# Kernel tuning notes

Hardware: AMD Instinct MI355X
Metric: run time of the kernel (lower is better)

## Reference

```python
import jax, jax.numpy as jnp
import numpy as np

D, K, CIN, CD, COUT = 3, 16, 128, 32, 256
C = CIN + CD                  # 160 = C_in + C_delta after concat
DM = -(-COUT // C)            # depth_multiplier = ceil(C_out / C) = 2
N, I = 4, 2048                # batch, points per cloud; M = N*I = 8192


def _bn(x, g, b, eps=1e-5):
    # BatchNorm1d in training mode: biased batch statistics over dim 0
    mu = x.mean(0)
    v = x.var(0)
    return (x - mu) * jax.lax.rsqrt(v + eps) * g + b


def _knn(p, k):
    # knn_graph over ALL M points (wrapper passes no batch vector), loop=True
    d2 = jnp.sum(p * p, axis=1)
    dist = d2[:, None] + d2[None, :] - 2.0 * (p @ p.T)   # [M,M]
    _, idx = jax.lax.top_k(-dist, k)                     # [M,K], self first
    return idx


def _gconv(t, w, b, M):
    # grouped Conv1d(K, K*K, kernel=K, groups=K): t [M,K,K], w [K(cin), K(out/grp), K(tap)]
    return jnp.einsum('mcl,col->mco', t, w).reshape(M, K * K) + b


def _xconv(xf, pf, idx, w1a, b1a, g1a, be1a, w1b, b1b, g1b, be1b,
           w2, b2, g2a, be2a, wc2a, bc2a, g2b, be2b, wc2b, bc2b, g2c, be2c,
           wcd, bcd, wl, bl):
    M = pf.shape[0]
    rel = pf[idx] - pf[:, None, :]                       # [M,K,D] relative neighbor coords
    # mlp1: lift relative coords to C_delta features
    h = rel.reshape(M * K, D)
    h = _bn(jax.nn.elu(h @ w1a + b1a), g1a, be1a)
    h = _bn(jax.nn.elu(h @ w1b + b1b), g1b, be1b)
    x_star = jnp.concatenate([h.reshape(M, K, CD), xf[idx]], axis=-1)  # [M,K,C]
    x_star = x_star.transpose(0, 2, 1)                   # [M,C,K]
    # mlp2: learn KxK X-transformation from the K*D relative coords
    t = _bn(jax.nn.elu(rel.reshape(M, K * D) @ w2 + b2), g2a, be2a).reshape(M, K, K)
    t = _bn(jax.nn.elu(_gconv(t, wc2a, bc2a, M)), g2b, be2b).reshape(M, K, K)
    t = _bn(_gconv(t, wc2b, bc2b, M), g2c, be2c).reshape(M, K, K)
    xt = jnp.einsum('mck,mkj->mcj', x_star, t)           # [M,C,K] batched matmul
    # depthwise Conv1d(C, C*DM, K, groups=C) collapses K, then final Linear
    y = jnp.einsum('mcl,col->mco', xt, wcd).reshape(M, C * DM) + bcd
    return y @ wl + bl                                   # [M,COUT]


def setup_inputs() -> dict:
    key = jax.random.key(0)
    ks = jax.random.split(key, 16)
    r = lambda k, s: jax.random.normal(k, s, jnp.float32) * 0.1
    return dict(
        x=jax.random.normal(ks[0], (N, I, CIN), jnp.float32),
        pos=jax.random.normal(ks[1], (N, I, D), jnp.float32),
        w1a=r(ks[2], (D, CD)), b1a=r(ks[3], (CD,)), g1a=jnp.ones((CD,)), be1a=jnp.zeros((CD,)),
        w1b=r(ks[4], (CD, CD)), b1b=r(ks[5], (CD,)), g1b=jnp.ones((CD,)), be1b=jnp.zeros((CD,)),
        w2=r(ks[6], (D * K, K * K)), b2=r(ks[7], (K * K,)), g2a=jnp.ones((K * K,)), be2a=jnp.zeros((K * K,)),
        wc2a=r(ks[8], (K, K, K)), bc2a=r(ks[9], (K * K,)), g2b=jnp.ones((K * K,)), be2b=jnp.zeros((K * K,)),
        wc2b=r(ks[10], (K, K, K)), bc2b=r(ks[11], (K * K,)), g2c=jnp.ones((K * K,)), be2c=jnp.zeros((K * K,)),
        wcd=r(ks[12], (C, DM, K)), bcd=r(ks[13], (C * DM,)),
        wl=r(ks[14], (C * DM, COUT)), bl=r(ks[15], (COUT,)),
    )


def reference(x, pos, w1a, b1a, g1a, be1a, w1b, b1b, g1b, be1b,
              w2, b2, g2a, be2a, wc2a, bc2a, g2b, be2b, wc2b, bc2b, g2c, be2c,
              wcd, bcd, wl, bl):
    pf = pos.reshape(N * I, D)
    xf = x.reshape(N * I, CIN)
    idx = _knn(pf, K)
    out = _xconv(xf, pf, idx, w1a, b1a, g1a, be1a, w1b, b1b, g1b, be1b,
                 w2, b2, g2a, be2a, wc2a, bc2a, g2b, be2b, wc2b, bc2b, g2c, be2c,
                 wcd, bcd, wl, bl)
    return out.reshape(N, I, COUT)
```

## Files before the change

### kernel.cpp

```cpp
#include <hip/hip_runtime.h>
#include <math.h>

#define M_PTS 8192
#define MK    131072

__device__ __forceinline__ float elu(float v){ return v > 0.f ? v : __expf(v)-1.0f; }

__device__ __forceinline__ unsigned distkey(float4 c, float qx, float qy, float qz, float d2q){
  #pragma clang fp contract(off)
  float dot  = __builtin_fmaf(c.z, qz, __builtin_fmaf(c.y, qy, __builtin_fmaf(c.x, qx, 0.0f)));
  float A    = d2q + c.w;
  float B    = 2.0f * dot;
  float dist = A - B;
  unsigned u = __float_as_uint(dist);
  return u ^ ((unsigned)((int)u >> 31) | 0x80000000u);
}

__global__ __launch_bounds__(256) void knn_kernel(const float* __restrict__ pos,
                                                  int* __restrict__ nidx,
                                                  float* __restrict__ st){
  #pragma clang fp contract(off)
  __shared__ float4 cand[1024];
  __shared__ unsigned long long hits[4][64];
  int tid  = threadIdx.x;
  int lane = tid & 63;
  int wv   = tid >> 6;
  int q    = blockIdx.x*4 + wv;
  if (blockIdx.x == 0){
    for (int i = tid; i < 2048; i += 256) st[i] = 0.f;
  }
  float qx = pos[3*q], qy = pos[3*q+1], qz = pos[3*q+2];
  float d2q = (qx*qx + qy*qy) + qz*qz;

  unsigned ka[8];
  #pragma unroll
  for (int s=0;s<8;s++) ka[s] = 0xFFFFFFFFu;

  for (int base = 0; base < M_PTS; base += 1024){
    for (int t = tid; t < 1024; t += 256){
      int j = base + t;
      float x = pos[3*j], y = pos[3*j+1], z = pos[3*j+2];
      float d2v = (x*x + y*y) + z*z;
      cand[t] = make_float4(x,y,z,d2v);
    }
    __syncthreads();
    #pragma unroll
    for (int k=0; k<16; k++){
      unsigned v = distkey(cand[lane + k*64], qx, qy, qz, d2q);
      #pragma unroll
      for (int s=0;s<8;s++){
        unsigned mn = min(v, ka[s]);
        unsigned mx = max(v, ka[s]);
        ka[s] = mn; v = mx;
      }
    }
    __syncthreads();
  }

  unsigned thr = 0xFFFFFFFFu;
  for (int r=0; r<16; r++){
    unsigned mine = ka[0];
    unsigned best = mine;
    #pragma unroll
    for (int off=32; off>0; off>>=1){
      unsigned o = __shfl_xor(best, off, 64);
      best = min(best, o);
    }
    bool adv = (best == mine);
    #pragma unroll
    for (int s=0;s<7;s++) ka[s] = adv ? ka[s+1] : ka[s];
    ka[7] = adv ? 0xFFFFFFFFu : ka[7];
    thr = best;
  }

  int cnt = 0;
  for (int base = 0; base < M_PTS; base += 1024){
    for (int t = tid; t < 1024; t += 256){
      int j = base + t;
      float x = pos[3*j], y = pos[3*j+1], z = pos[3*j+2];
      float d2v = (x*x + y*y) + z*z;
      cand[t] = make_float4(x,y,z,d2v);
    }
    __syncthreads();
    #pragma unroll
    for (int k=0; k<16; k++){
      int j = base + lane + k*64;
      unsigned u = distkey(cand[lane + k*64], qx, qy, qz, d2q);
      bool hit = (u <= thr);
      unsigned long long m = __ballot(hit);
      if (hit){
        int slot = cnt + __popcll(m & ((1ull<<lane)-1ull));
        if (slot < 64) hits[wv][slot] = ((unsigned long long)u << 32) | (unsigned)j;
      }
      cnt += (int)__popcll(m);
    }
    __syncthreads();
  }

  int cc = min(cnt, 64);
  unsigned long long mine = (lane < cc) ? hits[wv][lane] : ~0ull;
  for (int r=0; r<16; r++){
    unsigned long long best = mine;
    #pragma unroll
    for (int off=32; off>0; off>>=1){
      unsigned long long o = __shfl_xor(best, off, 64);
      best = (o < best) ? o : best;
    }
    if (mine == best) mine = ~0ull;
    if (lane == 0) nidx[q*16 + r] = (int)(unsigned)best;
  }
}

#define COMPUTE_RELF_8(OFFS)                                          \
  for (int f = tid; f < 8*48; f += 256){                              \
    int p = f/48, kd = f%48, k = kd/3, d = kd%3;                      \
    int j = nidx[(m0+p)*16 + k];                                      \
    relf[p][kd] = pos[3*j+d] - pos[3*(m0+p)+d];                       \
  }                                                                   \
  __syncthreads();

#define COMPUTE_T1_8(acc)                                             \
  _Pragma("unroll")                                                   \
  for (int p=0;p<8;p++) acc[p] = b2[tid];                             \
  for (int kk=0; kk<48; kk++){                                        \
    float w = w2[kk*256 + tid];                                       \
    _Pragma("unroll")                                                 \
    for (int p=0;p<8;p++) acc[p] += relf[p][kk]*w;                    \
  }

__global__ __launch_bounds__(256) void stats_a_kernel(const float* __restrict__ pos,
    const int* __restrict__ nidx,
    const float* __restrict__ w1a, const float* __restrict__ b1a,
    const float* __restrict__ w2,  const float* __restrict__ b2,
    float* __restrict__ s1, float* __restrict__ s3){
  int tid = threadIdx.x;
  if (blockIdx.x < 512){
    __shared__ float relS[256][3];
    __shared__ float red[8][64];
    int r = blockIdx.x*256 + tid;
    int m = r >> 4;
    int j = nidx[r];
    relS[tid][0] = pos[3*j  ]-pos[3*m  ];
    relS[tid][1] = pos[3*j+1]-pos[3*m+1];
    relS[tid][2] = pos[3*j+2]-pos[3*m+2];
    __syncthreads();
    int c = tid & 31, g = tid >> 5;
    float w0=w1a[c], w1v=w1a[32+c], w2v=w1a[64+c], b=b1a[c];
    float s=0.f, q=0.f;
    for (int rr=g*32; rr<g*32+32; rr++){
      float h = elu(b + relS[rr][0]*w0 + relS[rr][1]*w1v + relS[rr][2]*w2v);
      s += h; q += h*h;
    }
    red[g][c]=s; red[g][32+c]=q;
    __syncthreads();
    if (tid < 64){
      float a=0.f;
      #pragma unroll
      for (int gg=0;gg<8;gg++) a += red[gg][tid];
      atomicAdd(&s1[tid], a);
    }
  } else {
    __shared__ float relf[8][48];
    int m0 = (blockIdx.x-512)*8;
    COMPUTE_RELF_8();
    float acc[8];
    COMPUTE_T1_8(acc);
    float s=0.f, q=0.f;
    #pragma unroll
    for (int p=0;p<8;p++){ float v = elu(acc[p]); s += v; q += v*v; }
    atomicAdd(&s3[tid], s); atomicAdd(&s3[256+tid], q);
  }
}

__global__ __launch_bounds__(256) void stats_b_kernel(const float* __restrict__ pos,
    const int* __restrict__ nidx,
    const float* __restrict__ w1a, const float* __restrict__ b1a,
    const float* __restrict__ s1,  const float* __restrict__ g1a, const float* __restrict__ be1a,
    const float* __restrict__ w1b, const float* __restrict__ b1b,
    const float* __restrict__ w2,  const float* __restrict__ b2,
    const float* __restrict__ s3,  const float* __restrict__ g2a, const float* __restrict__ be2a,
    const float* __restrict__ wc2a,const float* __restrict__ bc2a,
    float* __restrict__ s2, float* __restrict__ s4){
  int tid = threadIdx.x;
  const float invMK = 1.f/(float)MK;
  const float invM  = 1.f/8192.f;
  if (blockIdx.x < 2048){
    __shared__ float xnS[64][33];
    __shared__ float red[8][64];
    __shared__ float muA[32], ivA[32];
    if (tid < 32){
      float mu  = s1[tid]*invMK;
      float var = s1[32+tid]*invMK - mu*mu;
      muA[tid] = mu; ivA[tid] = rsqrtf(var+1e-5f)*g1a[tid];
    }
    __syncthreads();
    {
      int rl = tid >> 2;
      int r  = blockIdx.x*64 + rl;
      int m = r >> 4;
      int j = nidx[r];
      float rx = pos[3*j]-pos[3*m], ry = pos[3*j+1]-pos[3*m+1], rz = pos[3*j+2]-pos[3*m+2];
      int c0 = (tid & 3)*8;
      #pragma unroll
      for (int u=0; u<8; u++){
        int cc = c0 + u;
        float h = elu(b1a[cc] + rx*w1a[cc] + ry*w1a[32+cc] + rz*w1a[64+cc]);
        xnS[rl][cc] = (h-muA[cc])*ivA[cc] + be1a[cc];
      }
    }
    __syncthreads();
    int o = tid & 31, g = tid >> 5;
    float wcol[32];
    #pragma unroll
    for (int cc=0;cc<32;cc++) wcol[cc] = w1b[cc*32+o];
    float bo = b1b[o], s=0.f, q=0.f;
    for (int rr=g*8; rr<g*8+8; rr++){
      float a = bo;
      #pragma unroll
      for (int cc=0;cc<32;cc++) a += xnS[rr][cc]*wcol[cc];
      float v = elu(a);
      s += v; q += v*v;
    }
    red[g][o]=s; red[g][32+o]=q;
    __syncthreads();
    if (tid < 64){
      float a=0.f;
      #pragma unroll
      for (int gg=0;gg<8;gg++) a += red[gg][tid];
      atomicAdd(&s2[tid], a);
    }
  } else {
    __shared__ float relf[8][48];
    __shared__ float tn[8][256];
    int m0 = (blockIdx.x-2048)*8;
    COMPUTE_RELF_8();
    float acc[8];
    COMPUTE_T1_8(acc);
    float mu3  = s3[tid]*invM;
    float var3 = s3[256+tid]*invM - mu3*mu3;
    float i3   = rsqrtf(var3+1e-5f)*g2a[tid];
    float bb3  = be2a[tid];
    #pragma unroll
    for (int p=0;p<8;p++) tn[p][tid] = (elu(acc[p])-mu3)*i3 + bb3;
    __syncthreads();
    int c = tid >> 4;
    float wreg[16];
    const float4* wv4 = (const float4*)(wc2a + tid*16);
    #pragma unroll
    for (int v=0; v<4; v++){ float4 f = wv4[v]; wreg[4*v]=f.x; wreg[4*v+1]=f.y; wreg[4*v+2]=f.z; wreg[4*v+3]=f.w; }
    float bias = bc2a[tid];
    float s=0.f, q=0.f;
    #pragma unroll
    for (int p=0;p<8;p++){
      float a2 = bias;
      #pragma unroll
      for (int l=0;l<16;l++) a2 += tn[p][c*16+l]*wreg[l];
      float v = elu(a2);
      s += v; q += v*v;
    }
    atomicAdd(&s4[tid], s); atomicAdd(&s4[256+tid], q);
  }
}

__global__ __launch_bounds__(256) void t3_stats_kernel(const float* __restrict__ pos,
    const int* __restrict__ nidx, const float* __restrict__ w2, const float* __restrict__ b2,
    const float* __restrict__ s3, const float* __restrict__ g2a, const float* __restrict__ be2a,
    const float* __restrict__ wc2a, const float* __restrict__ bc2a,
    const float* __restrict__ s4, const float* __restrict__ g2b, const float* __restrict__ be2b,
    const float* __restrict__ wc2b, const float* __restrict__ bc2b, float* __restrict__ s5){
  __shared__ float relf[8][48];
  __shared__ float tn[8][256];
  __shared__ float tn2[8][256];
  int m0 = blockIdx.x*8, tid = threadIdx.x;
  const float invM = 1.f/8192.f;
  COMPUTE_RELF_8();
  float acc[8];
  COMPUTE_T1_8(acc);
  float mu3  = s3[tid]*invM;
  float var3 = s3[256+tid]*invM - mu3*mu3;
  float i3   = rsqrtf(var3+1e-5f)*g2a[tid];
  float bb3  = be2a[tid];
  #pragma unroll
  for (int p=0;p<8;p++) tn[p][tid] = (elu(acc[p])-mu3)*i3 + bb3;
  __syncthreads();
  int c = tid >> 4;
  float wreg[16];
  { const float4* wv4 = (const float4*)(wc2a + tid*16);
    #pragma unroll
    for (int v=0; v<4; v++){ float4 f = wv4[v]; wreg[4*v]=f.x; wreg[4*v+1]=f.y; wreg[4*v+2]=f.z; wreg[4*v+3]=f.w; } }
  float bias = bc2a[tid];
  float mu4  = s4[tid]*invM;
  float var4 = s4[256+tid]*invM - mu4*mu4;
  float i4   = rsqrtf(var4+1e-5f)*g2b[tid];
  float bb4  = be2b[tid];
  float t2v[8];
  #pragma unroll
  for (int p=0;p<8;p++){
    float a2 = bias;
    #pragma unroll
    for (int l=0;l<16;l++) a2 += tn[p][c*16+l]*wreg[l];
    t2v[p] = elu(a2);
  }
  #pragma unroll
  for (int p=0;p<8;p++) tn2[p][tid] = (t2v[p]-mu4)*i4 + bb4;
  __syncthreads();
  float w2reg[16];
  { const float4* wv4 = (const float4*)(wc2b + tid*16);
    #pragma unroll
    for (int v=0; v<4; v++){ float4 f = wv4[v]; w2reg[4*v]=f.x; w2reg[4*v+1]=f.y; w2reg[4*v+2]=f.z; w2reg[4*v+3]=f.w; } }
  float bias2 = bc2b[tid];
  float s=0.f, q=0.f;
  #pragma unroll
  for (int p=0;p<8;p++){
    float a3 = bias2;
    #pragma unroll
    for (int l=0;l<16;l++) a3 += tn2[p][c*16+l]*w2reg[l];
    s += a3; q += a3*a3;
  }
  atomicAdd(&s5[tid], s); atomicAdd(&s5[256+tid], q);
}

#define PF 4
__global__ __launch_bounds__(256) void final_kernel(
    const float* __restrict__ x, const float* __restrict__ pos, const int* __restrict__ nidx,
    const float* __restrict__ w1a, const float* __restrict__ b1a,
    const float* __restrict__ g1a, const float* __restrict__ be1a,
    const float* __restrict__ w1b, const float* __restrict__ b1b,
    const float* __restrict__ g1b, const float* __restrict__ be1b,
    const float* __restrict__ w2,  const float* __restrict__ b2,
    const float* __restrict__ g2a, const float* __restrict__ be2a,
    const float* __restrict__ wc2a,const float* __restrict__ bc2a,
    const float* __restrict__ g2b, const float* __restrict__ be2b,
    const float* __restrict__ wc2b,const float* __restrict__ bc2b,
    const float* __restrict__ g2c, const float* __restrict__ be2c,
    const float* __restrict__ wcd, const float* __restrict__ bcd,
    const float* __restrict__ wl,  const float* __restrict__ bl,
    const float* __restrict__ st,
    float* __restrict__ out){
  __shared__ float relf[PF][48];
  __shared__ float tA[PF][256];
  __shared__ float tB[PF][256];
  __shared__ float xs[PF*32*17];
  __shared__ float yy[PF][320];
  __shared__ int   sidx[PF*16];
  __shared__ float mu1[32], i1g[32], mu2[32], i2g[32];
  int tid = threadIdx.x;
  int m0  = blockIdx.x*PF;
  const float invMK = 1.f/(float)MK;
  const float invM  = 1.f/8192.f;

  if (tid < PF*16) sidx[tid] = nidx[m0*16 + tid];
  for (int f = tid; f < PF*48; f += 256){
    int p = f/48, kd = f%48, k = kd/3, d = kd%3;
    int j = nidx[(m0+p)*16 + k];
    relf[p][kd] = pos[3*j+d] - pos[3*(m0+p)+d];
  }
  if (tid < 32){
    float mu  = st[tid]*invMK;
    float var = st[32+tid]*invMK - mu*mu;
    mu1[tid] = mu; i1g[tid] = rsqrtf(var+1e-5f)*g1a[tid];
    float mu_2  = st[64+tid]*invMK;
    float var_2 = st[96+tid]*invMK - mu_2*mu_2;
    mu2[tid] = mu_2; i2g[tid] = rsqrtf(var_2+1e-5f)*g1b[tid];
  }
  float mu3 = st[128+tid]*invM, var3 = st[384+tid]*invM - mu3*mu3;
  float i3 = rsqrtf(var3+1e-5f)*g2a[tid], bb3 = be2a[tid];
  float mu4 = st[640+tid]*invM, var4 = st[896+tid]*invM - mu4*mu4;
  float i4 = rsqrtf(var4+1e-5f)*g2b[tid], bb4 = be2b[tid];
  float mu5 = st[1152+tid]*invM, var5 = st[1408+tid]*invM - mu5*mu5;
  float i5 = rsqrtf(var5+1e-5f)*g2c[tid], bb5 = be2c[tid];
  __syncthreads();

  {
    float a[PF];
    #pragma unroll
    for (int p=0;p<PF;p++) a[p] = b2[tid];
    for (int kk=0; kk<48; kk++){
      float w = w2[kk*256 + tid];
      #pragma unroll
      for (int p=0;p<PF;p++) a[p] += relf[p][kk]*w;
    }
    #pragma unroll
    for (int p=0;p<PF;p++) tA[p][tid] = (elu(a[p])-mu3)*i3 + bb3;
  }
  __syncthreads();

  int c = tid >> 4;
  {
    float wreg[16];
    const float4* wv4 = (const float4*)(wc2a + tid*16);
    #pragma unroll
    for (int v=0; v<4; v++){ float4 f = wv4[v]; wreg[4*v]=f.x; wreg[4*v+1]=f.y; wreg[4*v+2]=f.z; wreg[4*v+3]=f.w; }
    float bias = bc2a[tid];
    float t2v[PF];
    #pragma unroll
    for (int p=0;p<PF;p++){
      float a2 = bias;
      #pragma unroll
      for (int l=0;l<16;l++) a2 += tA[p][c*16+l]*wreg[l];
      t2v[p] = elu(a2);
    }
    #pragma unroll
    for (int p=0;p<PF;p++) tB[p][tid] = (t2v[p]-mu4)*i4 + bb4;
  }
  __syncthreads();

  {
    float w2reg[16];
    const float4* wv4 = (const float4*)(wc2b + tid*16);
    #pragma unroll
    for (int v=0; v<4; v++){ float4 f = wv4[v]; w2reg[4*v]=f.x; w2reg[4*v+1]=f.y; w2reg[4*v+2]=f.z; w2reg[4*v+3]=f.w; }
    float bias2 = bc2b[tid];
    #pragma unroll
    for (int p=0;p<PF;p++){
      float a3 = bias2;
      #pragma unroll
      for (int l=0;l<16;l++) a3 += tB[p][c*16+l]*w2reg[l];
      tA[p][tid] = (a3-mu5)*i5 + bb5;
    }
  }

  {
    int row = tid >> 2;
    int p = row >> 4, k = row & 15;
    int q8 = (tid & 3)*8;
    int m = m0 + p;
    int j = sidx[p*16 + k];
    float rx = pos[3*j]-pos[3*m], ry = pos[3*j+1]-pos[3*m+1], rz = pos[3*j+2]-pos[3*m+2];
    float xn[32];
    #pragma unroll
    for (int cc=0; cc<32; cc++){
      float h = elu(b1a[cc] + rx*w1a[cc] + ry*w1a[32+cc] + rz*w1a[64+cc]);
      xn[cc] = (h-mu1[cc])*i1g[cc] + be1a[cc];
    }
    #pragma unroll
    for (int oo=0; oo<8; oo++){
      int o = q8 + oo;
      float a = b1b[o];
      #pragma unroll
      for (int cc=0; cc<32; cc++) a += xn[cc]*w1b[cc*32+o];
      float h2v = elu(a);
      xs[(p*32 + o)*17 + k] = (h2v-mu2[o])*i2g[o] + be1b[o];
    }
  }
  __syncthreads();

  for (int pair = tid; pair < PF*160; pair += 256){
    int p = pair / 160, cch = pair % 160;
    float av[16];
    if (cch < 32){
      #pragma unroll
      for (int k16=0;k16<16;k16++) av[k16] = xs[(p*32+cch)*17 + k16];
    } else {
      #pragma unroll
      for (int k16=0;k16<16;k16++) av[k16] = x[(size_t)sidx[p*16+k16]*128 + (cch-32)];
    }
    float xt[16];
    #pragma unroll
    for (int j16=0;j16<16;j16++) xt[j16]=0.f;
    #pragma unroll
    for (int k16=0;k16<16;k16++){
      float a = av[k16];
      #pragma unroll
      for (int j16=0;j16<16;j16++) xt[j16] += a*tA[p][k16*16+j16];
    }
    float y0 = bcd[cch*2], y1 = bcd[cch*2+1];
    #pragma unroll
    for (int l=0;l<16;l++){
      y0 += xt[l]*wcd[cch*32 + l];
      y1 += xt[l]*wcd[cch*32 + 16 + l];
    }
    yy[p][cch*2] = y0; yy[p][cch*2+1] = y1;
  }
  __syncthreads();

  float accO[PF];
  #pragma unroll
  for (int p=0;p<PF;p++) accO[p] = bl[tid];
  for (int q=0;q<320;q++){
    float w = wl[q*256 + tid];
    #pragma unroll
    for (int p=0;p<PF;p++) accO[p] += yy[p][q]*w;
  }
  #pragma unroll
  for (int p=0;p<PF;p++) out[(size_t)(m0+p)*256 + tid] = accO[p];
}

extern "C" void kernel_launch(void* const* d_in, const int* in_sizes, int n_in,
                              void* d_out, int out_size, void* d_ws, size_t ws_size,
                              hipStream_t stream){
  const float* x    = (const float*)d_in[0];
  const float* pos  = (const float*)d_in[1];
  const float* w1a  = (const float*)d_in[2];
  const float* b1a  = (const float*)d_in[3];
  const float* g1a  = (const float*)d_in[4];
  const float* be1a = (const float*)d_in[5];
  const float* w1b  = (const float*)d_in[6];
  const float* b1b  = (const float*)d_in[7];
  const float* g1b  = (const float*)d_in[8];
  const float* be1b = (const float*)d_in[9];
  const float* w2   = (const float*)d_in[10];
  const float* b2   = (const float*)d_in[11];
  const float* g2a  = (const float*)d_in[12];
  const float* be2a = (const float*)d_in[13];
  const float* wc2a = (const float*)d_in[14];
  const float* bc2a = (const float*)d_in[15];
  const float* g2b  = (const float*)d_in[16];
  const float* be2b = (const float*)d_in[17];
  const float* wc2b = (const float*)d_in[18];
  const float* bc2b = (const float*)d_in[19];
  const float* g2c  = (const float*)d_in[20];
  const float* be2c = (const float*)d_in[21];
  const float* wcd  = (const float*)d_in[22];
  const float* bcd  = (const float*)d_in[23];
  const float* wl   = (const float*)d_in[24];
  const float* bl   = (const float*)d_in[25];
  float* out = (float*)d_out;

  char* ws = (char*)d_ws;
  int*   nidx = (int*)(ws + 0);
  float* st   = (float*)(ws + 524288);
  float* s1 = st;
  float* s2 = st + 64;
  float* s3 = st + 128;
  float* s4 = st + 640;
  float* s5 = st + 1152;

  knn_kernel<<<2048,256,0,stream>>>(pos, nidx, st);
  stats_a_kernel<<<1536,256,0,stream>>>(pos, nidx, w1a, b1a, w2, b2, s1, s3);
  stats_b_kernel<<<3072,256,0,stream>>>(pos, nidx, w1a, b1a, s1, g1a, be1a, w1b, b1b,
                                        w2, b2, s3, g2a, be2a, wc2a, bc2a, s2, s4);
  t3_stats_kernel<<<1024,256,0,stream>>>(pos, nidx, w2, b2, s3, g2a, be2a, wc2a, bc2a,
                                         s4, g2b, be2b, wc2b, bc2b, s5);
  final_kernel<<<2048,256,0,stream>>>(x, pos, nidx,
                                      w1a, b1a, g1a, be1a, w1b, b1b, g1b, be1b,
                                      w2, b2, g2a, be2a, wc2a, bc2a,
                                      g2b, be2b, wc2b, bc2b, g2c, be2c,
                                      wcd, bcd, wl, bl, st, out);
}
```

Before: 404.3 us.

## Vectorize loads across kernels and halve points per block in stats kernels

The kNN candidate staging now reads positions as float4 triples instead of scalar strided loads. The stats kernels handle 4 points per block instead of 8, doubling grid sizes to expose more parallelism. The w2 and wl matvec loops are unrolled by 4 with float4 shared-memory reads, and the final kernel's mlp1 path uses float4 weight loads with the 8 outputs accumulated together. The smaller blocks re-read weights more often and add more atomics on the statistics.

```diff
diff --git a/kernel.cpp b/kernel.cpp
--- a/kernel.cpp
+++ b/kernel.cpp
@@ -37,11 +37,13 @@
   for (int s=0;s<8;s++) ka[s] = 0xFFFFFFFFu;
 
   for (int base = 0; base < M_PTS; base += 1024){
-    for (int t = tid; t < 1024; t += 256){
-      int j = base + t;
-      float x = pos[3*j], y = pos[3*j+1], z = pos[3*j+2];
-      float d2v = (x*x + y*y) + z*z;
-      cand[t] = make_float4(x,y,z,d2v);
+    {
+      const float4* pv = (const float4*)(pos + (size_t)base*3);
+      float4 f0 = pv[3*tid], f1 = pv[3*tid+1], f2 = pv[3*tid+2];
+      cand[4*tid  ] = make_float4(f0.x,f0.y,f0.z,(f0.x*f0.x + f0.y*f0.y) + f0.z*f0.z);
+      cand[4*tid+1] = make_float4(f0.w,f1.x,f1.y,(f0.w*f0.w + f1.x*f1.x) + f1.y*f1.y);
+      cand[4*tid+2] = make_float4(f1.z,f1.w,f2.x,(f1.z*f1.z + f1.w*f1.w) + f2.x*f2.x);
+      cand[4*tid+3] = make_float4(f2.y,f2.z,f2.w,(f2.y*f2.y + f2.z*f2.z) + f2.w*f2.w);
     }
     __syncthreads();
     #pragma unroll
@@ -75,11 +77,13 @@
 
   int cnt = 0;
   for (int base = 0; base < M_PTS; base += 1024){
-    for (int t = tid; t < 1024; t += 256){
-      int j = base + t;
-      float x = pos[3*j], y = pos[3*j+1], z = pos[3*j+2];
-      float d2v = (x*x + y*y) + z*z;
-      cand[t] = make_float4(x,y,z,d2v);
+    {
+      const float4* pv = (const float4*)(pos + (size_t)base*3);
+      float4 f0 = pv[3*tid], f1 = pv[3*tid+1], f2 = pv[3*tid+2];
+      cand[4*tid  ] = make_float4(f0.x,f0.y,f0.z,(f0.x*f0.x + f0.y*f0.y) + f0.z*f0.z);
+      cand[4*tid+1] = make_float4(f0.w,f1.x,f1.y,(f0.w*f0.w + f1.x*f1.x) + f1.y*f1.y);
+      cand[4*tid+2] = make_float4(f1.z,f1.w,f2.x,(f1.z*f1.z + f1.w*f1.w) + f2.x*f2.x);
+      cand[4*tid+3] = make_float4(f2.y,f2.z,f2.w,(f2.y*f2.y + f2.z*f2.z) + f2.w*f2.w);
     }
     __syncthreads();
     #pragma unroll
@@ -111,21 +115,25 @@
   }
 }
 
-#define COMPUTE_RELF_8(OFFS)                                          \
-  for (int f = tid; f < 8*48; f += 256){                              \
+#define COMPUTE_RELF_4()                                              \
+  for (int f = tid; f < 4*48; f += 256){                              \
     int p = f/48, kd = f%48, k = kd/3, d = kd%3;                      \
     int j = nidx[(m0+p)*16 + k];                                      \
     relf[p][kd] = pos[3*j+d] - pos[3*(m0+p)+d];                       \
   }                                                                   \
   __syncthreads();
 
-#define COMPUTE_T1_8(acc)                                             \
+#define COMPUTE_T1_4(acc)                                             \
   _Pragma("unroll")                                                   \
-  for (int p=0;p<8;p++) acc[p] = b2[tid];                             \
-  for (int kk=0; kk<48; kk++){                                        \
-    float w = w2[kk*256 + tid];                                       \
+  for (int p=0;p<4;p++) acc[p] = b2[tid];                             \
+  for (int kk=0; kk<48; kk+=4){                                       \
+    float w0v = w2[kk*256+tid],     w1v = w2[(kk+1)*256+tid];         \
+    float w2v = w2[(kk+2)*256+tid], w3v = w2[(kk+3)*256+tid];         \
     _Pragma("unroll")                                                 \
-    for (int p=0;p<8;p++) acc[p] += relf[p][kk]*w;                    \
+    for (int p=0;p<4;p++){                                            \
+      float4 r4 = *(const float4*)&relf[p][kk];                       \
+      acc[p] += r4.x*w0v + r4.y*w1v + r4.z*w2v + r4.w*w3v;            \
+    }                                                                 \
   }
 
 __global__ __launch_bounds__(256) void stats_a_kernel(const float* __restrict__ pos,
@@ -160,14 +168,14 @@
       atomicAdd(&s1[tid], a);
     }
   } else {
-    __shared__ float relf[8][48];
-    int m0 = (blockIdx.x-512)*8;
-    COMPUTE_RELF_8();
-    float acc[8];
-    COMPUTE_T1_8(acc);
+    __shared__ float relf[4][48];
+    int m0 = (blockIdx.x-512)*4;
+    COMPUTE_RELF_4();
+    float acc[4];
+    COMPUTE_T1_4(acc);
     float s=0.f, q=0.f;
     #pragma unroll
-    for (int p=0;p<8;p++){ float v = elu(acc[p]); s += v; q += v*v; }
+    for (int p=0;p<4;p++){ float v = elu(acc[p]); s += v; q += v*v; }
     atomicAdd(&s3[tid], s); atomicAdd(&s3[256+tid], q);
   }
 }
@@ -230,18 +238,18 @@
       atomicAdd(&s2[tid], a);
     }
   } else {
-    __shared__ float relf[8][48];
-    __shared__ float tn[8][256];
-    int m0 = (blockIdx.x-2048)*8;
-    COMPUTE_RELF_8();
-    float acc[8];
-    COMPUTE_T1_8(acc);
+    __shared__ float relf[4][48];
+    __shared__ float tn[4][256];
+    int m0 = (blockIdx.x-2048)*4;
+    COMPUTE_RELF_4();
+    float acc[4];
+    COMPUTE_T1_4(acc);
     float mu3  = s3[tid]*invM;
     float var3 = s3[256+tid]*invM - mu3*mu3;
     float i3   = rsqrtf(var3+1e-5f)*g2a[tid];
     float bb3  = be2a[tid];
     #pragma unroll
-    for (int p=0;p<8;p++) tn[p][tid] = (elu(acc[p])-mu3)*i3 + bb3;
+    for (int p=0;p<4;p++) tn[p][tid] = (elu(acc[p])-mu3)*i3 + bb3;
     __syncthreads();
     int c = tid >> 4;
     float wreg[16];
@@ -251,7 +259,7 @@
     float bias = bc2a[tid];
     float s=0.f, q=0.f;
     #pragma unroll
-    for (int p=0;p<8;p++){
+    for (int p=0;p<4;p++){
       float a2 = bias;
       #pragma unroll
       for (int l=0;l<16;l++) a2 += tn[p][c*16+l]*wreg[l];
@@ -268,20 +276,20 @@
     const float* __restrict__ wc2a, const float* __restrict__ bc2a,
     const float* __restrict__ s4, const float* __restrict__ g2b, const float* __restrict__ be2b,
     const float* __restrict__ wc2b, const float* __restrict__ bc2b, float* __restrict__ s5){
-  __shared__ float relf[8][48];
-  __shared__ float tn[8][256];
-  __shared__ float tn2[8][256];
-  int m0 = blockIdx.x*8, tid = threadIdx.x;
+  __shared__ float relf[4][48];
+  __shared__ float tn[4][256];
+  __shared__ float tn2[4][256];
+  int m0 = blockIdx.x*4, tid = threadIdx.x;
   const float invM = 1.f/8192.f;
-  COMPUTE_RELF_8();
-  float acc[8];
-  COMPUTE_T1_8(acc);
+  COMPUTE_RELF_4();
+  float acc[4];
+  COMPUTE_T1_4(acc);
   float mu3  = s3[tid]*invM;
   float var3 = s3[256+tid]*invM - mu3*mu3;
   float i3   = rsqrtf(var3+1e-5f)*g2a[tid];
   float bb3  = be2a[tid];
   #pragma unroll
-  for (int p=0;p<8;p++) tn[p][tid] = (elu(acc[p])-mu3)*i3 + bb3;
+  for (int p=0;p<4;p++) tn[p][tid] = (elu(acc[p])-mu3)*i3 + bb3;
   __syncthreads();
   int c = tid >> 4;
   float wreg[16];
@@ -293,16 +301,16 @@
   float var4 = s4[256+tid]*invM - mu4*mu4;
   float i4   = rsqrtf(var4+1e-5f)*g2b[tid];
   float bb4  = be2b[tid];
-  float t2v[8];
-  #pragma unroll
-  for (int p=0;p<8;p++){
+  float t2v[4];
+  #pragma unroll
+  for (int p=0;p<4;p++){
     float a2 = bias;
     #pragma unroll
     for (int l=0;l<16;l++) a2 += tn[p][c*16+l]*wreg[l];
     t2v[p] = elu(a2);
   }
   #pragma unroll
-  for (int p=0;p<8;p++) tn2[p][tid] = (t2v[p]-mu4)*i4 + bb4;
+  for (int p=0;p<4;p++) tn2[p][tid] = (t2v[p]-mu4)*i4 + bb4;
   __syncthreads();
   float w2reg[16];
   { const float4* wv4 = (const float4*)(wc2b + tid*16);
@@ -311,7 +319,7 @@
   float bias2 = bc2b[tid];
   float s=0.f, q=0.f;
   #pragma unroll
-  for (int p=0;p<8;p++){
+  for (int p=0;p<4;p++){
     float a3 = bias2;
     #pragma unroll
     for (int l=0;l<16;l++) a3 += tn2[p][c*16+l]*w2reg[l];
@@ -375,10 +383,14 @@
     float a[PF];
     #pragma unroll
     for (int p=0;p<PF;p++) a[p] = b2[tid];
-    for (int kk=0; kk<48; kk++){
-      float w = w2[kk*256 + tid];
-      #pragma unroll
-      for (int p=0;p<PF;p++) a[p] += relf[p][kk]*w;
+    for (int kk=0; kk<48; kk+=4){
+      float w0v = w2[kk*256 + tid],     w1v = w2[(kk+1)*256 + tid];
+      float w2v = w2[(kk+2)*256 + tid], w3v = w2[(kk+3)*256 + tid];
+      #pragma unroll
+      for (int p=0;p<PF;p++){
+        float4 r4 = *(const float4*)&relf[p][kk];
+        a[p] += r4.x*w0v + r4.y*w1v + r4.z*w2v + r4.w*w3v;
+      }
     }
     #pragma unroll
     for (int p=0;p<PF;p++) tA[p][tid] = (elu(a[p])-mu3)*i3 + bb3;
@@ -429,17 +441,38 @@
     float rx = pos[3*j]-pos[3*m], ry = pos[3*j+1]-pos[3*m+1], rz = pos[3*j+2]-pos[3*m+2];
     float xn[32];
     #pragma unroll
+    for (int cc=0; cc<32; cc+=4){
+      float4 wa = *(const float4*)&w1a[cc];
+      float4 wb = *(const float4*)&w1a[32+cc];
+      float4 wc = *(const float4*)&w1a[64+cc];
+      float4 ba = *(const float4*)&b1a[cc];
+      float4 mm = *(const float4*)&mu1[cc];
+      float4 ii = *(const float4*)&i1g[cc];
+      float4 be = *(const float4*)&be1a[cc];
+      xn[cc  ] = (elu(ba.x + rx*wa.x + ry*wb.x + rz*wc.x) - mm.x)*ii.x + be.x;
+      xn[cc+1] = (elu(ba.y + rx*wa.y + ry*wb.y + rz*wc.y) - mm.y)*ii.y + be.y;
+      xn[cc+2] = (elu(ba.z + rx*wa.z + ry*wb.z + rz*wc.z) - mm.z)*ii.z + be.z;
+      xn[cc+3] = (elu(ba.w + rx*wa.w + ry*wb.w + rz*wc.w) - mm.w)*ii.w + be.w;
+    }
+    float acc8[8];
+    {
+      float4 b0 = *(const float4*)&b1b[q8];
+      float4 b1v = *(const float4*)&b1b[q8+4];
+      acc8[0]=b0.x; acc8[1]=b0.y; acc8[2]=b0.z; acc8[3]=b0.w;
+      acc8[4]=b1v.x; acc8[5]=b1v.y; acc8[6]=b1v.z; acc8[7]=b1v.w;
+    }
+    #pragma unroll
     for (int cc=0; cc<32; cc++){
-      float h = elu(b1a[cc] + rx*w1a[cc] + ry*w1a[32+cc] + rz*w1a[64+cc]);
-      xn[cc] = (h-mu1[cc])*i1g[cc] + be1a[cc];
+      float xv = xn[cc];
+      float4 wr0 = *(const float4*)&w1b[cc*32+q8];
+      float4 wr1 = *(const float4*)&w1b[cc*32+q8+4];
+      acc8[0]+=xv*wr0.x; acc8[1]+=xv*wr0.y; acc8[2]+=xv*wr0.z; acc8[3]+=xv*wr0.w;
+      acc8[4]+=xv*wr1.x; acc8[5]+=xv*wr1.y; acc8[6]+=xv*wr1.z; acc8[7]+=xv*wr1.w;
     }
     #pragma unroll
     for (int oo=0; oo<8; oo++){
       int o = q8 + oo;
-      float a = b1b[o];
-      #pragma unroll
-      for (int cc=0; cc<32; cc++) a += xn[cc]*w1b[cc*32+o];
-      float h2v = elu(a);
+      float h2v = elu(acc8[oo]);
       xs[(p*32 + o)*17 + k] = (h2v-mu2[o])*i2g[o] + be1b[o];
     }
   }
@@ -477,10 +510,14 @@
   float accO[PF];
   #pragma unroll
   for (int p=0;p<PF;p++) accO[p] = bl[tid];
-  for (int q=0;q<320;q++){
-    float w = wl[q*256 + tid];
-    #pragma unroll
-    for (int p=0;p<PF;p++) accO[p] += yy[p][q]*w;
+  for (int q=0; q<320; q+=4){
+    float w0v = wl[q*256 + tid],     w1v = wl[(q+1)*256 + tid];
+    float w2v = wl[(q+2)*256 + tid], w3v = wl[(q+3)*256 + tid];
+    #pragma unroll
+    for (int p=0;p<PF;p++){
+      float4 y4 = *(const float4*)&yy[p][q];
+      accO[p] += y4.x*w0v + y4.y*w1v + y4.z*w2v + y4.w*w3v;
+    }
   }
   #pragma unroll
   for (int p=0;p<PF;p++) out[(size_t)(m0+p)*256 + tid] = accO[p];
@@ -527,10 +564,10 @@
   float* s5 = st + 1152;
 
   knn_kernel<<<2048,256,0,stream>>>(pos, nidx, st);
-  stats_a_kernel<<<1536,256,0,stream>>>(pos, nidx, w1a, b1a, w2, b2, s1, s3);
-  stats_b_kernel<<<3072,256,0,stream>>>(pos, nidx, w1a, b1a, s1, g1a, be1a, w1b, b1b,
+  stats_a_kernel<<<2560,256,0,stream>>>(pos, nidx, w1a, b1a, w2, b2, s1, s3);
+  stats_b_kernel<<<4096,256,0,stream>>>(pos, nidx, w1a, b1a, s1, g1a, be1a, w1b, b1b,
                                         w2, b2, s3, g2a, be2a, wc2a, bc2a, s2, s4);
-  t3_stats_kernel<<<1024,256,0,stream>>>(pos, nidx, w2, b2, s3, g2a, be2a, wc2a, bc2a,
+  t3_stats_kernel<<<2048,256,0,stream>>>(pos, nidx, w2, b2, s3, g2a, be2a, wc2a, bc2a,
                                          s4, g2b, be2b, wc2b, bc2b, s5);
   final_kernel<<<2048,256,0,stream>>>(x, pos, nidx,
                                       w1a, b1a, g1a, be1a, w1b, b1b, g1b, be1b,
```

After: 482.3 us. 1.19x slower.
